# Optimization experiments

Hardware: AMD Instinct MI355X
Metric: run time of the kernel (lower is better)

Reference implementation:

```python
import jax, jax.numpy as jnp
import numpy as np

N = 100_000   # nodes
E = 1_600_000 # edges per graph
D = 64        # feature width
HA = 32       # attention hidden


def setup_inputs() -> dict:
    key = jax.random.key(0)
    ks = jax.random.split(key, 20)
    inp = {}
    inp["h"] = jax.random.normal(ks[0], (N, D), jnp.float32)
    inp["e_od"] = jax.random.normal(ks[1], (E, D), jnp.float32)
    inp["e_ad"] = jax.random.normal(ks[2], (E, D), jnp.float32)
    inp["src_od"] = jax.random.randint(ks[3], (E,), 0, N)
    inp["dst_od"] = jax.random.randint(ks[4], (E,), 0, N)
    inp["src_ad"] = jax.random.randint(ks[5], (E,), 0, N)
    inp["dst_ad"] = jax.random.randint(ks[6], (E,), 0, N)
    s = 1.0 / np.sqrt(D).astype(np.float32)
    # stacked params: index 0 = OD graph, index 1 = AD graph
    inp["W_src"]  = jax.random.normal(ks[7],  (2, D, D), jnp.float32) * s
    inp["W_dst"]  = jax.random.normal(ks[8],  (2, D, D), jnp.float32) * s
    inp["W_edge"] = jax.random.normal(ks[9],  (2, D, D), jnp.float32) * s
    inp["b_msg"]  = jnp.zeros((2, D), jnp.float32)
    inp["W_self"] = jax.random.normal(ks[10], (2, D, D), jnp.float32) * s
    inp["W_agg"]  = jax.random.normal(ks[11], (2, D, D), jnp.float32) * s
    inp["b_node"] = jnp.zeros((2, D), jnp.float32)
    # Attention (Aggregate_samedim): Linear(D->HA, bias) -> tanh -> Linear(HA->1, no bias)
    inp["attn_l1_w"] = jax.random.normal(ks[12], (D, HA), jnp.float32) * s
    inp["attn_l1_b"] = jnp.zeros((HA,), jnp.float32)
    inp["attn_l2_w"] = jax.random.normal(ks[13], (HA, 1), jnp.float32) * (1.0 / np.sqrt(HA).astype(np.float32))
    return inp


def reference(h, e_od, e_ad, src_od, dst_od, src_ad, dst_ad,
              W_src, W_dst, W_edge, b_msg, W_self, W_agg, b_node,
              attn_l1_w, attn_l1_b, attn_l2_w):
    def mpnn(i, e, src, dst):
        # edge message: gather src/dst node feats, small GEMMs, relu  [E, D]
        m = jax.nn.relu(h[src] @ W_src[i] + h[dst] @ W_dst[i] + e @ W_edge[i] + b_msg[i])
        # scatter-sum to destination nodes  [N, D]
        agg = jax.ops.segment_sum(m, dst, num_segments=N)
        # node update  [N, D]
        return jax.nn.relu(h @ W_self[i] + agg @ W_agg[i] + b_node[i])

    intra = mpnn(0, e_od, src_od, dst_od)  # OD graph node states
    inter = mpnn(1, e_ad, src_ad, dst_ad)  # AD graph node states
    # Aggregate_samedim: attention over the 2-way stack
    rep = jnp.stack([intra, inter], axis=1)               # [N, 2, D]
    w = jnp.tanh(rep @ attn_l1_w + attn_l1_b) @ attn_l2_w  # [N, 2, 1]
    beta = jax.nn.softmax(w, axis=1)
    return (beta * rep).sum(axis=1)                        # [N, D]
```

## Files before the change

### kernel.cpp

```cpp
#include <hip/hip_runtime.h>
#include <hip/hip_bf16.h>

using short8  = __attribute__((ext_vector_type(8))) short;
using ushort8 = __attribute__((ext_vector_type(8))) unsigned short;
using f32x4   = __attribute__((ext_vector_type(4))) float;
using fvec4   = __attribute__((ext_vector_type(4))) float;

#define CH 8192

__device__ inline unsigned short f2bf(float x) {
  union { __hip_bfloat16 b; unsigned short u; } c;
  c.b = __float2bfloat16(x);
  return c.u;
}
__device__ inline float bf2f(unsigned short s) {
  return __uint_as_float(((unsigned int)s) << 16);
}
__device__ inline unsigned int pk2(float lo, float hi) {
  union { __hip_bfloat162 b; unsigned int u; } c;
  c.b = __float22bfloat162_rn(make_float2(lo, hi));
  return c.u;
}
__device__ inline short8 cvt8(fvec4 a, fvec4 b) {
  union { short8 s; unsigned int u[4]; } r;
  r.u[0] = pk2(a[0], a[1]);
  r.u[1] = pk2(a[2], a[3]);
  r.u[2] = pk2(b[0], b[1]);
  r.u[3] = pk2(b[2], b[3]);
  return r.s;
}

__device__ inline void load_bfrags_f32(const float* __restrict__ W, short8 bfr[2][4], int lane) {
  int l15 = lane & 15, lh = lane >> 4;
#pragma unroll
  for (int ks = 0; ks < 2; ++ks)
#pragma unroll
    for (int ct = 0; ct < 4; ++ct) {
      short8 v;
#pragma unroll
      for (int i = 0; i < 8; ++i)
        v[i] = (short)f2bf(W[(ks * 32 + lh * 8 + i) * 64 + ct * 16 + l15]);
      bfr[ks][ct] = v;
    }
}

__device__ inline void load_bfrags(const unsigned short* __restrict__ Wf, short8 bfr[2][4], int lane) {
#pragma unroll
  for (int ks = 0; ks < 2; ++ks)
#pragma unroll
    for (int ct = 0; ct < 4; ++ct) {
      union { ushort8 u; short8 s; } c;
      c.u = *reinterpret_cast<const ushort8*>(Wf + (((ks * 4 + ct) << 9) + (lane << 3)));
      bfr[ks][ct] = c.s;
    }
}

struct PrepArgs {
  const float* W[10];
};

__global__ __launch_bounds__(64) void prep_w_kernel(PrepArgs pw, unsigned short* __restrict__ Wf) {
  int z = blockIdx.x;
  int lane = threadIdx.x & 63;
  short8 bfr[2][4];
  load_bfrags_f32(pw.W[z], bfr, lane);
  unsigned short* dst = Wf + (size_t)z * 4096;
#pragma unroll
  for (int ks = 0; ks < 2; ++ks)
#pragma unroll
    for (int ct = 0; ct < 4; ++ct) {
      union { short8 s; ushort8 u; } c;
      c.s = bfr[ks][ct];
      *reinterpret_cast<ushort8*>(dst + (((ks * 4 + ct) << 9) + (lane << 3))) = c.u;
    }
}

struct ProjArgs {
  unsigned short* out[6];
};

__global__ __launch_bounds__(256) void proj_all_kernel(const float* __restrict__ h,
                                                       const unsigned short* __restrict__ Wf,
                                                       ProjArgs pa, int N) {
  int lane = threadIdx.x & 63;
  int wv = threadIdx.x >> 6;
  int rowbase = blockIdx.x * 256 + wv * 64;
  int l15 = lane & 15, lh = lane >> 4;

  short8 afr[4][2];
#pragma unroll
  for (int rt = 0; rt < 4; ++rt) {
    int row = rowbase + rt * 16 + l15;
    int rc = row < N ? row : 0;
    const fvec4* p = reinterpret_cast<const fvec4*>(h + (size_t)rc * 64);
#pragma unroll
    for (int ks = 0; ks < 2; ++ks)
      afr[rt][ks] = cvt8(p[ks * 8 + lh * 2], p[ks * 8 + lh * 2 + 1]);
  }

  for (int z = 0; z < 6; ++z) {
    short8 bfr[2][4];
    load_bfrags(Wf + (size_t)z * 4096, bfr, lane);
    unsigned short* __restrict__ out = pa.out[z];

    f32x4 acc[4][4];
#pragma unroll
    for (int rt = 0; rt < 4; ++rt)
#pragma unroll
      for (int ct = 0; ct < 4; ++ct) acc[rt][ct] = (f32x4){0.f, 0.f, 0.f, 0.f};

#pragma unroll
    for (int rt = 0; rt < 4; ++rt)
#pragma unroll
      for (int ks = 0; ks < 2; ++ks)
#pragma unroll
        for (int ct = 0; ct < 4; ++ct)
          acc[rt][ct] = __builtin_amdgcn_mfma_f32_16x16x32_bf16(afr[rt][ks], bfr[ks][ct], acc[rt][ct], 0, 0, 0);

#pragma unroll
    for (int rt = 0; rt < 4; ++rt)
#pragma unroll
      for (int rg = 0; rg < 4; ++rg) {
        int row = rowbase + rt * 16 + lh * 4 + rg;
        if (row < N) {
#pragma unroll
          for (int ct = 0; ct < 4; ++ct)
            out[(size_t)row * 64 + ct * 16 + l15] = f2bf(acc[rt][ct][rg]);
        }
      }
  }
}

__global__ __launch_bounds__(256) void hist_kernel(const int* __restrict__ dst0, const int* __restrict__ dst1,
                                                   int* __restrict__ counts, int E, int NBK) {
  __shared__ int hcnt[2048];
  int z = blockIdx.y;
  const int* __restrict__ dst = z ? dst1 : dst0;
  int t = threadIdx.x;
  for (int i = t; i < NBK; i += 256) hcnt[i] = 0;
  __syncthreads();
  int base = blockIdx.x * CH;
#pragma unroll 4
  for (int k = 0; k < CH / 256; ++k) {
    int i = base + k * 256 + t;
    if (i < E) atomicAdd(&hcnt[dst[i] >> 6], 1);
  }
  __syncthreads();
  for (int i = t; i < NBK; i += 256) {
    int c = hcnt[i];
    if (c) atomicAdd(&counts[(size_t)z * NBK + i], c);
  }
}

__global__ __launch_bounds__(1024) void scan_kernel(const int* __restrict__ counts, int* __restrict__ cursor,
                                                    int* __restrict__ gcur, int NBK) {
  int z = blockIdx.x;
  const int* c = counts + (size_t)z * NBK;
  __shared__ int lds[1024];
  int t = threadIdx.x;
  int carry = 0;
  for (int base = 0; base < NBK; base += 1024) {
    int i = base + t;
    int v = (i < NBK) ? c[i] : 0;
    lds[t] = v;
    __syncthreads();
    for (int off = 1; off < 1024; off <<= 1) {
      int x = (t >= off) ? lds[t - off] : 0;
      __syncthreads();
      lds[t] += x;
      __syncthreads();
    }
    if (i < NBK) {
      int excl = carry + lds[t] - v;
      cursor[(size_t)z * NBK + i] = excl;
      gcur[(size_t)z * NBK + i] = excl;
    }
    carry += lds[1023];
    __syncthreads();
  }
}

__global__ __launch_bounds__(256) void scatterA_kernel(
    const int* __restrict__ src0, const int* __restrict__ dst0,
    const int* __restrict__ src1, const int* __restrict__ dst1,
    int* __restrict__ gcur, int2* __restrict__ recs0, int2* __restrict__ recs1,
    int E, int NBK) {
  __shared__ int lcnt[2048];
  int z = blockIdx.y;
  const int* __restrict__ src = z ? src1 : src0;
  const int* __restrict__ dst = z ? dst1 : dst0;
  int2* __restrict__ recs = z ? recs1 : recs0;
  int t = threadIdx.x;
  for (int i = t; i < NBK; i += 256) lcnt[i] = 0;
  __syncthreads();
  int base = blockIdx.x * CH;
#pragma unroll 4
  for (int k = 0; k < CH / 256; ++k) {
    int i = base + k * 256 + t;
    if (i < E) atomicAdd(&lcnt[dst[i] >> 6], 1);
  }
  __syncthreads();
  for (int i = t; i < NBK; i += 256) {
    int c = lcnt[i];
    lcnt[i] = c ? atomicAdd(&gcur[(size_t)z * NBK + i], c) : 0;
  }
  __syncthreads();
#pragma unroll 4
  for (int k = 0; k < CH / 256; ++k) {
    int i = base + k * 256 + t;
    if (i < E) {
      int d = dst[i], s = src[i];
      int bin = d >> 6, dl = d & 63;
      int pos = atomicAdd(&lcnt[bin], 1);
      recs[pos] = make_int2(i | (bin << 21), s | (dl << 26));
    }
  }
}

__global__ __launch_bounds__(256) void sortB_kernel(int2* __restrict__ recs0, int2* __restrict__ recs1,
                                                    const int* __restrict__ cursor,
                                                    const int* __restrict__ counts, int NBK) {
  __shared__ int cnt_lds[64];
  __shared__ int cur_lds[64];
  int z = blockIdx.y;
  int b = blockIdx.x;
  int2* __restrict__ recs = z ? recs1 : recs0;
  int start = cursor[(size_t)z * NBK + b];
  int cnt = counts[(size_t)z * NBK + b];
  int t = threadIdx.x;

  for (int cbase = 0; cbase < cnt; cbase += 2048) {
    int ccnt = min(2048, cnt - cbase);
    int2 r[8];
    int dl[8];
    if (t < 64) cnt_lds[t] = 0;
    __syncthreads();
#pragma unroll
    for (int k = 0; k < 8; ++k) {
      int idx = k * 256 + t;
      if (idx < ccnt) {
        r[k] = recs[start + cbase + idx];
        dl[k] = ((unsigned)r[k].y) >> 26;
        atomicAdd(&cnt_lds[dl[k]], 1);
      }
    }
    __syncthreads();
    if (t < 64) {
      int c = cnt_lds[t];
      int x = c;
#pragma unroll
      for (int off = 1; off < 64; off <<= 1) {
        int y = __shfl_up(x, off);
        if (t >= off) x += y;
      }
      cur_lds[t] = x - c;
    }
    __syncthreads();
#pragma unroll
    for (int k = 0; k < 8; ++k) {
      int idx = k * 256 + t;
      if (idx < ccnt) {
        int pos = atomicAdd(&cur_lds[dl[k]], 1);
        recs[start + cbase + pos] = r[k];
      }
    }
    __syncthreads();
  }
}

struct EdgeArgs {
  const float* e[2];
  const int2* recs[2];
  const unsigned short* We[2];
  const float* bmsg[2];
  const unsigned short* Ps[2];
  const unsigned short* Pd[2];
  float* agg[2];
};

__global__ __launch_bounds__(256) void edge_sorted_kernel(EdgeArgs ea, int E) {
  __shared__ unsigned short x_lds[4][64 * 64];

  int z = blockIdx.y;
  const float* __restrict__ e = ea.e[z];
  const int2* __restrict__ recs = ea.recs[z];
  const unsigned short* __restrict__ Psrc = ea.Ps[z];
  const unsigned short* __restrict__ Pdst = ea.Pd[z];
  float* __restrict__ agg = ea.agg[z];

  int lane = threadIdx.x & 63;
  int wv = threadIdx.x >> 6;
  int base = (blockIdx.x * 4 + wv) * 64;
  if (base >= E) return;
  int l15 = lane & 15, lh = lane >> 4;
  unsigned short* xw = &x_lds[wv][0];

  int slot = base + lane;
  int el = 0, sl = 0, dl = 0;
  if (slot < E) {
    int2 rc = recs[slot];
    el = rc.x & 0x1FFFFF;
    sl = rc.y & 0x3FFFFFF;
    dl = (((rc.x >> 21) & 0x7FF) << 6) | (int)(((unsigned)rc.y) >> 26);
  }

  short8 bfr[2][4];
  load_bfrags(ea.We[z], bfr, lane);

  short8 idf[2];
#pragma unroll
  for (int half = 0; half < 2; ++half) {
    short8 v;
#pragma unroll
    for (int i = 0; i < 8; ++i)
      v[i] = (short)((lh * 8 + i == half * 16 + l15) ? 0x3F80 : 0);
    idf[half] = v;
  }

  const float* bmsg = ea.bmsg[z];
  f32x4 acc[4][4];
#pragma unroll
  for (int ct = 0; ct < 4; ++ct) {
    float b = bmsg[ct * 16 + l15];
    f32x4 bb = (f32x4){b, b, b, b};
#pragma unroll
    for (int rt = 0; rt < 4; ++rt) acc[rt][ct] = bb;
  }

#pragma unroll
  for (int rt = 0; rt < 4; ++rt) {
    int sr = rt * 16 + l15;
    int er = __shfl(el, sr);
    int hr = __shfl(sl, sr);
    const fvec4* pr = reinterpret_cast<const fvec4*>(e + ((size_t)er << 6));
    const ushort8* ps = reinterpret_cast<const ushort8*>(Psrc + ((size_t)hr << 6));
    short8 aE0 = cvt8(pr[lh * 2], pr[lh * 2 + 1]);
    short8 aE1 = cvt8(pr[8 + lh * 2], pr[8 + lh * 2 + 1]);
    union { ushort8 u; short8 s; } aP0, aP1;
    aP0.u = ps[lh];
    aP1.u = ps[4 + lh];
#pragma unroll
    for (int ct = 0; ct < 4; ++ct) {
      acc[rt][ct] = __builtin_amdgcn_mfma_f32_16x16x32_bf16(aE0, bfr[0][ct], acc[rt][ct], 0, 0, 0);
      acc[rt][ct] = __builtin_amdgcn_mfma_f32_16x16x32_bf16(aE1, bfr[1][ct], acc[rt][ct], 0, 0, 0);
    }
    acc[rt][0] = __builtin_amdgcn_mfma_f32_16x16x32_bf16(aP0.s, idf[0], acc[rt][0], 0, 0, 0);
    acc[rt][1] = __builtin_amdgcn_mfma_f32_16x16x32_bf16(aP0.s, idf[1], acc[rt][1], 0, 0, 0);
    acc[rt][2] = __builtin_amdgcn_mfma_f32_16x16x32_bf16(aP1.s, idf[0], acc[rt][2], 0, 0, 0);
    acc[rt][3] = __builtin_amdgcn_mfma_f32_16x16x32_bf16(aP1.s, idf[1], acc[rt][3], 0, 0, 0);
  }

#pragma unroll
  for (int rt = 0; rt < 4; ++rt)
#pragma unroll
    for (int ct = 0; ct < 4; ++ct) {
      int col = ct * 16 + l15;
      int byte = (col << 7) + ((rt * 32 + lh * 8) ^ ((col & 7) << 4));
      uint2 d;
      d.x = pk2(acc[rt][ct][0], acc[rt][ct][1]);
      d.y = pk2(acc[rt][ct][2], acc[rt][ct][3]);
      *reinterpret_cast<uint2*>(reinterpret_cast<char*>(xw) + byte) = d;
    }

  asm volatile("s_waitcnt lgkmcnt(0)" ::: "memory");
  __builtin_amdgcn_sched_barrier(0);

  ushort8 xv[8];
#pragma unroll
  for (int i = 0; i < 8; ++i) {
    int byte = (lane << 7) + ((i * 16) ^ ((lane & 7) << 4));
    xv[i] = *reinterpret_cast<ushort8*>(reinterpret_cast<char*>(xw) + byte);
  }

  int dprev = __shfl_up(dl, 1);
  unsigned long long bnd = __ballot(lane > 0 && dl != dprev);
  int vrows = min(64, E - base);

  float racc = 0.f, pdv = 0.f;
  int dcur = -1;
#pragma unroll
  for (int r = 0; r < 64; ++r) {
    bool newseg = (r == 0) || ((bnd >> r) & 1ull);
    if (newseg) {
      if (dcur >= 0) atomicAdd(&agg[(size_t)dcur * 64 + lane], racc);
      dcur = __shfl(dl, r);
      racc = 0.f;
      pdv = bf2f(Pdst[(size_t)dcur * 64 + lane]);
    }
    float v = fmaxf(bf2f(xv[r >> 3][r & 7]) + pdv, 0.f);
    racc += (r < vrows) ? v : 0.f;
  }
  if (dcur >= 0) atomicAdd(&agg[(size_t)dcur * 64 + lane], racc);
}

struct NodeArgs {
  const float* agg[2];
  const unsigned short* T[2];
  const float* bn[2];
  unsigned short* U[2];
};

__global__ __launch_bounds__(256) void node_kernel(const unsigned short* __restrict__ Wf,
                                                   NodeArgs na, int N) {
  int z = blockIdx.y;
  const float* __restrict__ agg = na.agg[z];
  const unsigned short* __restrict__ T = na.T[z];
  const float* __restrict__ bn = na.bn[z];
  unsigned short* __restrict__ U = na.U[z];
  int lane = threadIdx.x & 63;
  int wv = threadIdx.x >> 6;
  int rowbase = blockIdx.x * 256 + wv * 64;
  int l15 = lane & 15, lh = lane >> 4;

  short8 bfr[2][4];
  load_bfrags(Wf + (size_t)(8 + z) * 4096, bfr, lane);

  f32x4 acc[4][4];
#pragma unroll
  for (int rt = 0; rt < 4; ++rt)
#pragma unroll
    for (int ct = 0; ct < 4; ++ct) acc[rt][ct] = (f32x4){0.f, 0.f, 0.f, 0.f};

#pragma unroll
  for (int rt = 0; rt < 4; ++rt) {
    int row = rowbase + rt * 16 + l15;
    int rc = row < N ? row : 0;
    const fvec4* p = reinterpret_cast<const fvec4*>(agg + (size_t)rc * 64);
#pragma unroll
    for (int ks = 0; ks < 2; ++ks) {
      fvec4 p0 = p[ks * 8 + lh * 2], p1 = p[ks * 8 + lh * 2 + 1];
      short8 ahi = cvt8(p0, p1);
      fvec4 q0, q1;
#pragma unroll
      for (int i = 0; i < 4; ++i) {
        q0[i] = p0[i] - bf2f((unsigned short)ahi[i]);
        q1[i] = p1[i] - bf2f((unsigned short)ahi[i + 4]);
      }
      short8 alo = cvt8(q0, q1);
#pragma unroll
      for (int ct = 0; ct < 4; ++ct) {
        acc[rt][ct] = __builtin_amdgcn_mfma_f32_16x16x32_bf16(ahi, bfr[ks][ct], acc[rt][ct], 0, 0, 0);
        acc[rt][ct] = __builtin_amdgcn_mfma_f32_16x16x32_bf16(alo, bfr[ks][ct], acc[rt][ct], 0, 0, 0);
      }
    }
  }

  float bv[4];
#pragma unroll
  for (int ct = 0; ct < 4; ++ct) bv[ct] = bn[ct * 16 + l15];

#pragma unroll
  for (int rt = 0; rt < 4; ++rt)
#pragma unroll
    for (int rg = 0; rg < 4; ++rg) {
      int row = rowbase + rt * 16 + lh * 4 + rg;
      if (row < N) {
#pragma unroll
        for (int ct = 0; ct < 4; ++ct) {
          int c = ct * 16 + l15;
          float v = acc[rt][ct][rg] + bf2f(T[(size_t)row * 64 + c]) + bv[ct];
          U[(size_t)row * 64 + c] = f2bf(fmaxf(v, 0.0f));
        }
      }
    }
}

__global__ __launch_bounds__(256) void attn_kernel(
    const unsigned short* __restrict__ U0, const unsigned short* __restrict__ U1,
    const float* __restrict__ l1w, const float* __restrict__ l1b, const float* __restrict__ l2w,
    float* __restrict__ out, int N) {
  int t = threadIdx.x;
  int node = blockIdx.x * 64 + (t >> 2);
  int q = t & 3;
  if (node >= N) return;
  size_t b0 = (size_t)node * 64;

  float a0[8], a1[8];
#pragma unroll
  for (int i = 0; i < 8; ++i) { a0[i] = l1b[q * 8 + i]; a1[i] = a0[i]; }

  for (int k = 0; k < 64; ++k) {
    float u0 = bf2f(U0[b0 + k]);
    float u1 = bf2f(U1[b0 + k]);
#pragma unroll
    for (int i = 0; i < 8; ++i) {
      float w = l1w[k * 32 + q * 8 + i];
      a0[i] += u0 * w;
      a1[i] += u1 * w;
    }
  }
  float w0 = 0.f, w1 = 0.f;
#pragma unroll
  for (int i = 0; i < 8; ++i) {
    float l2 = l2w[q * 8 + i];
    w0 += tanhf(a0[i]) * l2;
    w1 += tanhf(a1[i]) * l2;
  }
  w0 += __shfl_xor(w0, 1, 4); w0 += __shfl_xor(w0, 2, 4);
  w1 += __shfl_xor(w1, 1, 4); w1 += __shfl_xor(w1, 2, 4);

  float m = fmaxf(w0, w1);
  float e0 = expf(w0 - m), e1 = expf(w1 - m);
  float inv = 1.0f / (e0 + e1);
  float be0 = e0 * inv, be1 = e1 * inv;

#pragma unroll
  for (int j = 0; j < 16; ++j) {
    int c = q * 16 + j;
    out[b0 + c] = be0 * bf2f(U0[b0 + c]) + be1 * bf2f(U1[b0 + c]);
  }
}

static inline size_t au(size_t x) { return (x + 255) & ~(size_t)255; }

extern "C" void kernel_launch(void* const* d_in, const int* in_sizes, int n_in,
                              void* d_out, int out_size, void* d_ws, size_t ws_size,
                              hipStream_t stream) {
  const float* h      = (const float*)d_in[0];
  const float* e_od   = (const float*)d_in[1];
  const float* e_ad   = (const float*)d_in[2];
  const int* src_od   = (const int*)d_in[3];
  const int* dst_od   = (const int*)d_in[4];
  const int* src_ad   = (const int*)d_in[5];
  const int* dst_ad   = (const int*)d_in[6];
  const float* W_src  = (const float*)d_in[7];
  const float* W_dst  = (const float*)d_in[8];
  const float* W_edge = (const float*)d_in[9];
  const float* b_msg  = (const float*)d_in[10];
  const float* W_self = (const float*)d_in[11];
  const float* W_agg  = (const float*)d_in[12];
  const float* b_node = (const float*)d_in[13];
  const float* l1w    = (const float*)d_in[14];
  const float* l1b    = (const float*)d_in[15];
  const float* l2w    = (const float*)d_in[16];
  float* out = (float*)d_out;

  int N = in_sizes[0] / 64;
  int E = in_sizes[1] / 64;
  int NBK = (N + 63) >> 6;

  char* ws = (char*)d_ws;
  size_t off = 0;
  int* counts = (int*)(ws + off);   off += au((size_t)2 * NBK * sizeof(int));
  float* agg0 = (float*)(ws + off); off += (size_t)N * 64 * sizeof(float);
  float* agg1 = (float*)(ws + off); off += (size_t)N * 64 * sizeof(float);
  size_t zero_bytes = off;
  int* cursor = (int*)(ws + off);   off += au((size_t)2 * NBK * sizeof(int));
  int* gcur   = (int*)(ws + off);   off += au((size_t)2 * NBK * sizeof(int));
  int2* recs0 = (int2*)(ws + off);  off += au((size_t)E * sizeof(int2));
  int2* recs1 = (int2*)(ws + off);  off += au((size_t)E * sizeof(int2));
  unsigned short* Wf = (unsigned short*)(ws + off); off += au((size_t)10 * 4096 * sizeof(unsigned short));
  size_t NP = au((size_t)N * 64 * sizeof(unsigned short));
  unsigned short* Psrc0 = (unsigned short*)(ws + off); off += NP;
  unsigned short* Pdst0 = (unsigned short*)(ws + off); off += NP;
  unsigned short* Psrc1 = (unsigned short*)(ws + off); off += NP;
  unsigned short* Pdst1 = (unsigned short*)(ws + off); off += NP;
  unsigned short* T0    = (unsigned short*)(ws + off); off += NP;
  unsigned short* T1    = (unsigned short*)(ws + off); off += NP;
  unsigned short* U0 = Psrc0;
  unsigned short* U1 = Psrc1;

  hipMemsetAsync(ws, 0, zero_bytes, stream);

  PrepArgs pw;
  pw.W[0] = W_src;         pw.W[1] = W_dst;
  pw.W[2] = W_src + 4096;  pw.W[3] = W_dst + 4096;
  pw.W[4] = W_self;        pw.W[5] = W_self + 4096;
  pw.W[6] = W_edge;        pw.W[7] = W_edge + 4096;
  pw.W[8] = W_agg;         pw.W[9] = W_agg + 4096;
  prep_w_kernel<<<10, 64, 0, stream>>>(pw, Wf);

  int nb = (N + 255) / 256;
  ProjArgs pa;
  pa.out[0] = Psrc0;
  pa.out[1] = Pdst0;
  pa.out[2] = Psrc1;
  pa.out[3] = Pdst1;
  pa.out[4] = T0;
  pa.out[5] = T1;
  proj_all_kernel<<<nb, 256, 0, stream>>>(h, Wf, pa, N);

  int nch = (E + CH - 1) / CH;
  hist_kernel<<<dim3(nch, 2), 256, 0, stream>>>(dst_od, dst_ad, counts, E, NBK);
  scan_kernel<<<2, 1024, 0, stream>>>(counts, cursor, gcur, NBK);
  scatterA_kernel<<<dim3(nch, 2), 256, 0, stream>>>(src_od, dst_od, src_ad, dst_ad, gcur,
                                                    recs0, recs1, E, NBK);
  sortB_kernel<<<dim3(NBK, 2), 256, 0, stream>>>(recs0, recs1, cursor, counts, NBK);

  int tiles = (E + 63) / 64;
  int eb = (tiles + 3) / 4;
  EdgeArgs ea;
  ea.e[0] = e_od;  ea.recs[0] = recs0; ea.We[0] = Wf + 6 * 4096; ea.bmsg[0] = b_msg;
  ea.Ps[0] = Psrc0; ea.Pd[0] = Pdst0; ea.agg[0] = agg0;
  ea.e[1] = e_ad;  ea.recs[1] = recs1; ea.We[1] = Wf + 7 * 4096; ea.bmsg[1] = b_msg + 64;
  ea.Ps[1] = Psrc1; ea.Pd[1] = Pdst1; ea.agg[1] = agg1;
  edge_sorted_kernel<<<dim3(eb, 2), 256, 0, stream>>>(ea, E);

  NodeArgs na;
  na.agg[0] = agg0; na.T[0] = T0; na.bn[0] = b_node;      na.U[0] = U0;
  na.agg[1] = agg1; na.T[1] = T1; na.bn[1] = b_node + 64; na.U[1] = U1;
  node_kernel<<<dim3(nb, 2), 256, 0, stream>>>(Wf, na, N);

  attn_kernel<<<(N + 63) / 64, 256, 0, stream>>>(U0, U1, l1w, l1b, l2w, out, N);
}
```

Before: 529.5 us.

## Fold dst projection into MFMA and reduce segments directly from accumulators

The destination-node projection is now gathered per edge row and added through extra MFMAs with the identity fragment, so ReLU is applied directly on the accumulators. The LDS transpose round-trip is removed and segments are summed straight from the MFMA accumulator layout with cross-lane shuffles. This drops LDS traffic and the 64-step serial per-row loop. In exchange it adds per-edge Pdst gathers instead of per-segment ones, and the reduction walks segments one at a time with shuffle reductions, so many short segments could cost more.

```diff
diff --git a/kernel.cpp b/kernel.cpp
--- a/kernel.cpp
+++ b/kernel.cpp
@@ -279,8 +279,6 @@
 };
 
 __global__ __launch_bounds__(256) void edge_sorted_kernel(EdgeArgs ea, int E) {
-  __shared__ unsigned short x_lds[4][64 * 64];
-
   int z = blockIdx.y;
   const float* __restrict__ e = ea.e[z];
   const int2* __restrict__ recs = ea.recs[z];
@@ -293,7 +291,6 @@
   int base = (blockIdx.x * 4 + wv) * 64;
   if (base >= E) return;
   int l15 = lane & 15, lh = lane >> 4;
-  unsigned short* xw = &x_lds[wv][0];
 
   int slot = base + lane;
   int el = 0, sl = 0, dl = 0;
@@ -332,13 +329,17 @@
     int sr = rt * 16 + l15;
     int er = __shfl(el, sr);
     int hr = __shfl(sl, sr);
+    int dr = __shfl(dl, sr);
     const fvec4* pr = reinterpret_cast<const fvec4*>(e + ((size_t)er << 6));
     const ushort8* ps = reinterpret_cast<const ushort8*>(Psrc + ((size_t)hr << 6));
+    const ushort8* pd = reinterpret_cast<const ushort8*>(Pdst + ((size_t)dr << 6));
     short8 aE0 = cvt8(pr[lh * 2], pr[lh * 2 + 1]);
     short8 aE1 = cvt8(pr[8 + lh * 2], pr[8 + lh * 2 + 1]);
-    union { ushort8 u; short8 s; } aP0, aP1;
+    union { ushort8 u; short8 s; } aP0, aP1, aD0, aD1;
     aP0.u = ps[lh];
     aP1.u = ps[4 + lh];
+    aD0.u = pd[lh];
+    aD1.u = pd[4 + lh];
 #pragma unroll
     for (int ct = 0; ct < 4; ++ct) {
       acc[rt][ct] = __builtin_amdgcn_mfma_f32_16x16x32_bf16(aE0, bfr[0][ct], acc[rt][ct], 0, 0, 0);
@@ -348,49 +349,63 @@
     acc[rt][1] = __builtin_amdgcn_mfma_f32_16x16x32_bf16(aP0.s, idf[1], acc[rt][1], 0, 0, 0);
     acc[rt][2] = __builtin_amdgcn_mfma_f32_16x16x32_bf16(aP1.s, idf[0], acc[rt][2], 0, 0, 0);
     acc[rt][3] = __builtin_amdgcn_mfma_f32_16x16x32_bf16(aP1.s, idf[1], acc[rt][3], 0, 0, 0);
+    acc[rt][0] = __builtin_amdgcn_mfma_f32_16x16x32_bf16(aD0.s, idf[0], acc[rt][0], 0, 0, 0);
+    acc[rt][1] = __builtin_amdgcn_mfma_f32_16x16x32_bf16(aD0.s, idf[1], acc[rt][1], 0, 0, 0);
+    acc[rt][2] = __builtin_amdgcn_mfma_f32_16x16x32_bf16(aD1.s, idf[0], acc[rt][2], 0, 0, 0);
+    acc[rt][3] = __builtin_amdgcn_mfma_f32_16x16x32_bf16(aD1.s, idf[1], acc[rt][3], 0, 0, 0);
   }
 
 #pragma unroll
   for (int rt = 0; rt < 4; ++rt)
 #pragma unroll
-    for (int ct = 0; ct < 4; ++ct) {
-      int col = ct * 16 + l15;
-      int byte = (col << 7) + ((rt * 32 + lh * 8) ^ ((col & 7) << 4));
-      uint2 d;
-      d.x = pk2(acc[rt][ct][0], acc[rt][ct][1]);
-      d.y = pk2(acc[rt][ct][2], acc[rt][ct][3]);
-      *reinterpret_cast<uint2*>(reinterpret_cast<char*>(xw) + byte) = d;
-    }
-
-  asm volatile("s_waitcnt lgkmcnt(0)" ::: "memory");
-  __builtin_amdgcn_sched_barrier(0);
-
-  ushort8 xv[8];
-#pragma unroll
-  for (int i = 0; i < 8; ++i) {
-    int byte = (lane << 7) + ((i * 16) ^ ((lane & 7) << 4));
-    xv[i] = *reinterpret_cast<ushort8*>(reinterpret_cast<char*>(xw) + byte);
-  }
+    for (int ct = 0; ct < 4; ++ct)
+#pragma unroll
+      for (int rg = 0; rg < 4; ++rg)
+        acc[rt][ct][rg] = fmaxf(acc[rt][ct][rg], 0.f);
 
   int dprev = __shfl_up(dl, 1);
   unsigned long long bnd = __ballot(lane > 0 && dl != dprev);
   int vrows = min(64, E - base);
 
-  float racc = 0.f, pdv = 0.f;
-  int dcur = -1;
-#pragma unroll
-  for (int r = 0; r < 64; ++r) {
-    bool newseg = (r == 0) || ((bnd >> r) & 1ull);
-    if (newseg) {
-      if (dcur >= 0) atomicAdd(&agg[(size_t)dcur * 64 + lane], racc);
-      dcur = __shfl(dl, r);
-      racc = 0.f;
-      pdv = bf2f(Pdst[(size_t)dcur * 64 + lane]);
-    }
-    float v = fmaxf(bf2f(xv[r >> 3][r & 7]) + pdv, 0.f);
-    racc += (r < vrows) ? v : 0.f;
-  }
-  if (dcur >= 0) atomicAdd(&agg[(size_t)dcur * 64 + lane], racc);
+  int r0 = 0;
+  while (r0 < vrows) {
+    unsigned long long rest = (r0 < 63) ? (bnd >> (r0 + 1)) : 0ull;
+    int r1 = rest ? (r0 + 1 + __builtin_ctzll(rest)) : 64;
+    if (r1 > vrows) r1 = vrows;
+    int dcur = __shfl(dl, r0);
+
+    float s0 = 0.f, s1 = 0.f, s2 = 0.f, s3 = 0.f;
+#pragma unroll
+    for (int rt = 0; rt < 4; ++rt) {
+      int rs = rt * 16;
+      if (r0 <= rs && r1 >= rs + 16) {
+#pragma unroll
+        for (int rg = 0; rg < 4; ++rg) {
+          s0 += acc[rt][0][rg];
+          s1 += acc[rt][1][rg];
+          s2 += acc[rt][2][rg];
+          s3 += acc[rt][3][rg];
+        }
+      } else if (r0 < rs + 16 && r1 > rs) {
+#pragma unroll
+        for (int rg = 0; rg < 4; ++rg) {
+          int row = rs + lh * 4 + rg;
+          bool in = (row >= r0) && (row < r1);
+          s0 += in ? acc[rt][0][rg] : 0.f;
+          s1 += in ? acc[rt][1][rg] : 0.f;
+          s2 += in ? acc[rt][2][rg] : 0.f;
+          s3 += in ? acc[rt][3][rg] : 0.f;
+        }
+      }
+    }
+    s0 += __shfl_xor(s0, 16); s0 += __shfl_xor(s0, 32);
+    s1 += __shfl_xor(s1, 16); s1 += __shfl_xor(s1, 32);
+    s2 += __shfl_xor(s2, 16); s2 += __shfl_xor(s2, 32);
+    s3 += __shfl_xor(s3, 16); s3 += __shfl_xor(s3, 32);
+    float mine = (lh == 0) ? s0 : (lh == 1) ? s1 : (lh == 2) ? s2 : s3;
+    atomicAdd(&agg[(size_t)dcur * 64 + lane], mine);
+    r0 = r1;
+  }
 }
 
 struct NodeArgs {
```

After: 587.8 us. 1.11x slower.
